# Kernel tuning notes

Measured on AMD Instinct MI355X. Metric: run time of the kernel, lower is better.

## Reference

```python
import jax, jax.numpy as jnp
import numpy as np
import math

D = 1024
H = 16
NEG = -10000.0


def _layernorm(x, g, b, eps=1e-6):
    mu = x.mean(-1, keepdims=True)
    var = ((x - mu) ** 2).mean(-1, keepdims=True)
    return (x - mu) / jnp.sqrt(var + eps) * g + b


def _gelu(x):
    return x * 0.5 * (1.0 + jax.lax.erf(x / math.sqrt(2.0)))


def _split_heads(x):
    N, L, _ = x.shape
    return x.reshape(N, L, H, D // H).transpose(0, 2, 1, 3)  # (N,H,L,d)


def _attention(q, k, v, mask):
    # q,k,v: (N,Lq/Lk,D); mask: (N,1,Lq,Lk) of 0/1 or None
    d = D // H
    qh, kh, vh = _split_heads(q), _split_heads(k), _split_heads(v)
    scores = jnp.einsum('bhqd,bhkd->bhqk', qh, kh) / math.sqrt(d)
    if mask is not None:
        scores = scores + (1.0 - mask) * NEG
    probs = jax.nn.softmax(scores, axis=-1)
    ctx = jnp.einsum('bhqk,bhkd->bhqd', probs, vh)
    N, _, Lq, _ = ctx.shape
    ctx = ctx.transpose(0, 2, 1, 3).reshape(N, Lq, D)
    return ctx, scores.mean(1)  # attention_vis = masked scaled scores averaged over heads


def setup_inputs() -> dict:
    key = jax.random.key(0)
    ks = jax.random.split(key, 16)
    N, Lt, Lv = 16, 512, 512
    w = lambda k: (jax.random.normal(k, (D, D), jnp.float32) * 0.02)
    inp = {
        'dec_hidden_states': jax.random.normal(ks[0], (N, Lt, D), jnp.float32),
        'dec_mask': jnp.ones((N, Lt), jnp.float32),
        'enc_outputs': jax.random.normal(ks[1], (N, Lv, D), jnp.float32),
        'sa_wq': w(ks[2]), 'sa_bq': jnp.zeros((D,), jnp.float32),
        'sa_wk': w(ks[3]), 'sa_bk': jnp.zeros((D,), jnp.float32),
        'sa_wv': w(ks[4]), 'sa_bv': jnp.zeros((D,), jnp.float32),
        'n1_g': jnp.ones((D,), jnp.float32), 'n1_b': jnp.zeros((D,), jnp.float32),
        'ca_wq': w(ks[5]), 'ca_bq': jnp.zeros((D,), jnp.float32),
        'ca_wk': w(ks[6]), 'ca_bk': jnp.zeros((D,), jnp.float32),
        'ca_wv': w(ks[7]), 'ca_bv': jnp.zeros((D,), jnp.float32),
        'n2_g': jnp.ones((D,), jnp.float32), 'n2_b': jnp.zeros((D,), jnp.float32),
        'int_w': w(ks[8]), 'int_b': jnp.zeros((D,), jnp.float32),
        'out_w': w(ks[9]), 'out_b': jnp.zeros((D,), jnp.float32),
        'out_g': jnp.ones((D,), jnp.float32), 'out_beta': jnp.zeros((D,), jnp.float32),
    }
    return inp


def reference(dec_hidden_states, dec_mask, enc_outputs,
              sa_wq, sa_bq, sa_wk, sa_bk, sa_wv, sa_bv, n1_g, n1_b,
              ca_wq, ca_bq, ca_wk, ca_bk, ca_wv, ca_bv, n2_g, n2_b,
              int_w, int_b, out_w, out_b, out_g, out_beta):
    x = dec_hidden_states
    N, Lt, _ = x.shape
    # causal + padding mask: (N,1,Lt) * tril(Lt,Lt) -> (N,Lt,Lt) -> (N,1,Lt,Lt)
    causal = jnp.tril(jnp.ones((Lt, Lt), x.dtype))
    self_mask = (dec_mask[:, None, :] * causal)[:, None, :, :]
    # self attention
    q = x @ sa_wq + sa_bq
    k = x @ sa_wk + sa_bk
    v = x @ sa_wv + sa_bv
    sa_ctx, _ = _attention(q, k, v, self_mask)
    h = _layernorm(sa_ctx + x, n1_g, n1_b)
    # cross attention (no mask)
    cq = h @ ca_wq + ca_bq
    ck = enc_outputs @ ca_wk + ca_bk
    cv = enc_outputs @ ca_wv + ca_bv
    ca_ctx, attention_vis = _attention(cq, ck, cv, None)
    h2 = _layernorm(h + ca_ctx, n2_g, n2_b)
    # intermediate (gelu FFN)
    inter = _gelu(h2 @ int_w + int_b)
    # Output: dense + residual(intermediate itself, as in original) + LayerNorm
    out = _layernorm(inter @ out_w + out_b + inter, out_g, out_beta)
    return out, attention_vis
```

## Files before the change

kernel.cpp:

```cpp
#include <hip/hip_runtime.h>
#include <hip/hip_bf16.h>
#include <math.h>

#define DDIM 1024
#define NH   16
#define LTOK 512
#define NBATCH 16

typedef unsigned short u16;
typedef unsigned short u16x8 __attribute__((ext_vector_type(8)));
typedef unsigned short u16x4 __attribute__((ext_vector_type(4)));
typedef __bf16 bf16x8 __attribute__((ext_vector_type(8)));
typedef float f32x4 __attribute__((ext_vector_type(4)));

typedef __attribute__((address_space(1))) void as1_void;
typedef __attribute__((address_space(3))) void as3_void;

__device__ __forceinline__ void llds16(const u16* g, u16* l) {
    __builtin_amdgcn_global_load_lds((as1_void*)g, (as3_void*)l, 16, 0, 0);
}

__device__ __forceinline__ float bf2f(u16 u) {
    unsigned v = ((unsigned)u) << 16;
    float f; __builtin_memcpy(&f, &v, 4); return f;
}
__device__ __forceinline__ u16 f2bf(float f) {
    unsigned u; __builtin_memcpy(&u, &f, 4);
    u += 0x7fffu + ((u >> 16) & 1u);
    return (u16)(u >> 16);
}

__global__ __launch_bounds__(256) void gemm_bt_kernel(
    const u16* __restrict__ A, int lda, long sA1, long sA2,
    const u16* __restrict__ B, int ldb, long sB1, long sB2,
    u16* __restrict__ C, float* __restrict__ Cf, int ldc, long sC1, long sC2,
    int M, int N, int K, int zdiv,
    const float* __restrict__ bias, float scale, int flags)
{
    __shared__ __align__(16) u16 As[2 * 128 * 32];
    __shared__ __align__(16) u16 Bs[2 * 128 * 32];
    const int BUF = 128 * 32;

    const int z  = blockIdx.y;
    const int zb = z / zdiv, zh = z - zb * zdiv;
    const u16* Ab = A + (long)zb * sA1 + (long)zh * sA2;
    const u16* Bb = B + (long)zb * sB1 + (long)zh * sB2;
    u16*   Cb  = C  ? C  + (long)zb * sC1 + (long)zh * sC2 : nullptr;
    float* Cfb = Cf ? Cf + (long)zb * sC1 + (long)zh * sC2 : nullptr;

    const int tilesN = (N + 127) >> 7;
    const int tilesM = (M + 127) >> 7;
    int tm, tn;
    if ((tilesM & 7) == 0) {
        const int xcd = blockIdx.x & 7, idx = blockIdx.x >> 3;
        const int mg  = tilesM >> 3;
        tm = ((idx % mg) << 3) | xcd;
        tn = idx / mg;
    } else {
        tm = blockIdx.x / tilesN;
        tn = blockIdx.x - tm * tilesN;
    }
    const int m0 = tm << 7, n0 = tn << 7;

    const int tid  = threadIdx.x;
    const int lane = tid & 63;
    const int wave = tid >> 6;
    const int wm = (wave & 1) << 6, wn = (wave >> 1) << 6;
    const int quad = lane >> 4, l16 = lane & 15;

    f32x4 acc[4][4];
#pragma unroll
    for (int i = 0; i < 4; i++)
#pragma unroll
        for (int j = 0; j < 4; j++) acc[i][j] = (f32x4){0.f, 0.f, 0.f, 0.f};

    const int lrA = (wave << 5) + (lane >> 2);
    const int lc  = (lane & 3) << 3;
    int ra0 = m0 + lrA;      if (ra0 > M - 1) ra0 = M - 1;
    int ra1 = m0 + lrA + 16; if (ra1 > M - 1) ra1 = M - 1;
    int rb0 = n0 + lrA;      if (rb0 > N - 1) rb0 = N - 1;
    int rb1 = n0 + lrA + 16; if (rb1 > N - 1) rb1 = N - 1;
    const u16* gA0 = Ab + (long)ra0 * lda + lc;
    const u16* gA1 = Ab + (long)ra1 * lda + lc;
    const u16* gB0 = Bb + (long)rb0 * ldb + lc;
    const u16* gB1 = Bb + (long)rb1 * ldb + lc;
    u16* lA0 = As + ((wave << 5) +  0) * 32;
    u16* lA1 = As + ((wave << 5) + 16) * 32;
    u16* lB0 = Bs + ((wave << 5) +  0) * 32;
    u16* lB1 = Bs + ((wave << 5) + 16) * 32;

    llds16(gA0, lA0);
    llds16(gA1, lA1);
    llds16(gB0, lB0);
    llds16(gB1, lB1);
    __syncthreads();

    int cur = 0;
    for (int k0 = 0; k0 < K; k0 += 32) {
        const int nxt = cur ^ 1;
        if (k0 + 32 < K) {
            llds16(gA0 + k0 + 32, lA0 + nxt * BUF);
            llds16(gA1 + k0 + 32, lA1 + nxt * BUF);
            llds16(gB0 + k0 + 32, lB0 + nxt * BUF);
            llds16(gB1 + k0 + 32, lB1 + nxt * BUF);
        }

        const u16* Ac = As + cur * BUF;
        const u16* Bc = Bs + cur * BUF;
        bf16x8 af[4], bfr[4];
#pragma unroll
        for (int t = 0; t < 4; t++)
            af[t] = *(const bf16x8*)(Ac + (wm + t * 16 + l16) * 32 + quad * 8);
#pragma unroll
        for (int t = 0; t < 4; t++)
            bfr[t] = *(const bf16x8*)(Bc + (wn + t * 16 + l16) * 32 + quad * 8);
#pragma unroll
        for (int i = 0; i < 4; i++)
#pragma unroll
            for (int j = 0; j < 4; j++)
                acc[i][j] = __builtin_amdgcn_mfma_f32_16x16x32_bf16(
                    af[i], bfr[j], acc[i][j], 0, 0, 0);

        __syncthreads();
        cur = nxt;
    }

#pragma unroll
    for (int j = 0; j < 4; j++) {
        int col  = n0 + wn + j * 16 + l16;
        int colc = col < N ? col : N - 1;
        float bv = bias ? bias[colc] : 0.f;
#pragma unroll
        for (int i = 0; i < 4; i++) {
#pragma unroll
            for (int r = 0; r < 4; r++) {
                int row = m0 + wm + i * 16 + quad * 4 + r;
                float v = acc[i][j][r] * scale + bv;
                if (flags & 1)
                    v = 0.5f * v * (1.f + erff(v * 0.70710678118654752f));
                if (row < M && col < N) {
                    if (Cfb) Cfb[(long)row * ldc + col] = v;
                    else     Cb [(long)row * ldc + col] = f2bf(v);
                }
            }
        }
    }
}

__global__ __launch_bounds__(256, 4) void flash_kernel(
    const u16* __restrict__ Q, const u16* __restrict__ K,
    const u16* __restrict__ VT, u16* __restrict__ O,
    const float* __restrict__ mask, int causal, int ldq, int ldk)
{
    __shared__ __align__(16) u16 Ks[128 * 72];
    __shared__ __align__(16) u16 Vs[64 * 136];
    const int tid  = threadIdx.x;
    const int wave = tid >> 6, lane = tid & 63;
    const int quad = lane >> 4, l16 = lane & 15;
    const int bh = blockIdx.x, qt = blockIdx.y, b = bh >> 4, h = bh & 15;
    const int qbase = qt * 64 + wave * 16;
    const int qrow  = qbase + l16;

    const u16* qp = Q + ((long)b * LTOK + qrow) * ldq + h * 64 + quad * 8;
    bf16x8 aq0 = *(const bf16x8*)(qp);
    bf16x8 aq1 = *(const bf16x8*)(qp + 32);

    f32x4 oacc[4];
#pragma unroll
    for (int jd = 0; jd < 4; jd++) oacc[jd] = (f32x4){0.f, 0.f, 0.f, 0.f};
    float m_st = -3.0e38f;
    float l_st = 0.f;

    const int krow = tid >> 3,       kcol = (tid & 7) << 3;
    const int vrow = tid >> 2,       vcol = (tid & 3) << 3;
    const u16* gK = K + ((long)b * LTOK + krow) * ldk + h * 64 + kcol;
    const u16* gV = VT + ((long)bh * 64 + vrow) * LTOK + vcol;

    const float C1    = 0.125f * 1.44269504088896340736f;
    const float NEGL2 = -10000.0f * 1.44269504088896340736f;

    const int nkt = causal ? ((qt * 64 + 63) >> 7) + 1 : (LTOK >> 7);

    u16x8 KR[4], VR[4];
#pragma unroll
    for (int i = 0; i < 4; i++) KR[i] = *(const u16x8*)(gK + (long)(i * 32) * ldk);
#pragma unroll
    for (int i = 0; i < 4; i++) VR[i] = *(const u16x8*)(gV + i * 32);
#pragma unroll
    for (int i = 0; i < 4; i++)
        *(u16x8*)(Ks + (i * 32 + krow) * 72 + kcol) = KR[i];
#pragma unroll
    for (int i = 0; i < 4; i++)
        *(u16x8*)(Vs + vrow * 136 + i * 32 + vcol) = VR[i];
    __syncthreads();

    for (int kt = 0; kt < nkt; kt++) {
        const int k0 = kt << 7;
        const bool more = (kt + 1 < nkt);

        if (more) {
            const int kn = k0 + 128;
#pragma unroll
            for (int i = 0; i < 4; i++)
                KR[i] = *(const u16x8*)(gK + (long)(kn + i * 32) * ldk);
#pragma unroll
            for (int i = 0; i < 4; i++)
                VR[i] = *(const u16x8*)(gV + kn + i * 32);
        }

        f32x4 s[8];
#pragma unroll
        for (int j = 0; j < 8; j++) {
            bf16x8 bk0 = *(const bf16x8*)(Ks + (j * 16 + l16) * 72 + quad * 8);
            bf16x8 bk1 = *(const bf16x8*)(Ks + (j * 16 + l16) * 72 + 32 + quad * 8);
            f32x4 z = (f32x4){0.f, 0.f, 0.f, 0.f};
            z = __builtin_amdgcn_mfma_f32_16x16x32_bf16(bk0, aq0, z, 0, 0, 0);
            s[j] = __builtin_amdgcn_mfma_f32_16x16x32_bf16(bk1, aq1, z, 0, 0, 0);
        }

        float tm0 = -3.0e38f, tm1 = -3.0e38f, tm2 = -3.0e38f, tm3 = -3.0e38f;
#pragma unroll
        for (int j = 0; j < 8; j++) {
            if (causal) {
                f32x4 m4 = *(const f32x4*)(mask + (long)b * LTOK + k0 + j * 16 + quad * 4);
#pragma unroll
                for (int r = 0; r < 4; r++) {
                    int key = k0 + j * 16 + quad * 4 + r;
                    float ad = (key <= qrow) ? fmaf(m4[r], -NEGL2, NEGL2) : NEGL2;
                    s[j][r] = fmaf(s[j][r], C1, ad);
                }
            } else {
#pragma unroll
                for (int r = 0; r < 4; r++) s[j][r] *= C1;
            }
            tm0 = fmaxf(tm0, s[j][0]); tm1 = fmaxf(tm1, s[j][1]);
            tm2 = fmaxf(tm2, s[j][2]); tm3 = fmaxf(tm3, s[j][3]);
        }
        float tmax = fmaxf(fmaxf(tm0, tm1), fmaxf(tm2, tm3));
        tmax = fmaxf(tmax, __shfl_xor(tmax, 16));
        tmax = fmaxf(tmax, __shfl_xor(tmax, 32));

        float mnew  = fmaxf(m_st, tmax);
        float alpha = __builtin_amdgcn_exp2f(m_st - mnew);
        m_st = mnew;

        float rs0 = 0.f, rs1 = 0.f, rs2 = 0.f, rs3 = 0.f;
        unsigned pk[8][2];
#pragma unroll
        for (int j = 0; j < 8; j++) {
            float p0 = __builtin_amdgcn_exp2f(s[j][0] - mnew);
            float p1 = __builtin_amdgcn_exp2f(s[j][1] - mnew);
            float p2 = __builtin_amdgcn_exp2f(s[j][2] - mnew);
            float p3 = __builtin_amdgcn_exp2f(s[j][3] - mnew);
            rs0 += p0; rs1 += p1; rs2 += p2; rs3 += p3;
            asm("v_cvt_pk_bf16_f32 %0, %1, %2" : "=v"(pk[j][0]) : "v"(p0), "v"(p1));
            asm("v_cvt_pk_bf16_f32 %0, %1, %2" : "=v"(pk[j][1]) : "v"(p2), "v"(p3));
        }
        float rsum = (rs0 + rs1) + (rs2 + rs3);
        rsum += __shfl_xor(rsum, 16);
        rsum += __shfl_xor(rsum, 32);
        l_st = l_st * alpha + rsum;

#pragma unroll
        for (int jd = 0; jd < 4; jd++) oacc[jd] *= alpha;

#pragma unroll
        for (int kk = 0; kk < 4; kk++) {
            unsigned wv[4] = { pk[2 * kk][0], pk[2 * kk][1],
                               pk[2 * kk + 1][0], pk[2 * kk + 1][1] };
            bf16x8 bp; __builtin_memcpy(&bp, wv, 16);
#pragma unroll
            for (int jd = 0; jd < 4; jd++) {
                const u16* vb = Vs + (jd * 16 + l16) * 136 + kk * 32 + quad * 4;
                u16 va[8];
                *(u16x4*)(va)     = *(const u16x4*)(vb);
                *(u16x4*)(va + 4) = *(const u16x4*)(vb + 16);
                bf16x8 av; __builtin_memcpy(&av, va, 16);
                oacc[jd] = __builtin_amdgcn_mfma_f32_16x16x32_bf16(av, bp, oacc[jd], 0, 0, 0);
            }
        }

        if (more) {
            __syncthreads();
#pragma unroll
            for (int i = 0; i < 4; i++)
                *(u16x8*)(Ks + (i * 32 + krow) * 72 + kcol) = KR[i];
#pragma unroll
            for (int i = 0; i < 4; i++)
                *(u16x8*)(Vs + vrow * 136 + i * 32 + vcol) = VR[i];
            __syncthreads();
        }
    }

    float linv = 1.f / l_st;
    long obase = ((long)b * LTOK + qrow) * DDIM + h * 64;
#pragma unroll
    for (int jd = 0; jd < 4; jd++) {
        u16x4 ov;
#pragma unroll
        for (int r = 0; r < 4; r++) ov[r] = f2bf(oacc[jd][r] * linv);
        *(u16x4*)(O + obase + jd * 16 + quad * 4) = ov;
    }
}

__global__ __launch_bounds__(256) void add_ln_kernel(
    const u16* __restrict__ a, const u16* __restrict__ b,
    const float* __restrict__ b32,
    const float* __restrict__ g, const float* __restrict__ bt,
    u16* __restrict__ o, float* __restrict__ of)
{
    long row = blockIdx.x;
    int tid = threadIdx.x;
    __shared__ float red[4];
    const u16* ar = a + row * DDIM;
    float xv[4]; float s = 0.f;
#pragma unroll
    for (int i = 0; i < 4; i++) {
        int c = tid + 256 * i;
        float sum = bf2f(ar[c]) + (b32 ? b32[row * DDIM + c] : bf2f(b[row * DDIM + c]));
        xv[i] = fminf(fmaxf(sum, -1.0e18f), 1.0e18f);
        s += xv[i];
    }
#pragma unroll
    for (int ofs = 32; ofs >= 1; ofs >>= 1) s += __shfl_xor(s, ofs);
    int wave = tid >> 6, lane = tid & 63;
    if (lane == 0) red[wave] = s;
    __syncthreads();
    float mu = (red[0] + red[1] + red[2] + red[3]) * (1.f / 1024.f);
    __syncthreads();
    float v = 0.f;
#pragma unroll
    for (int i = 0; i < 4; i++) { float d = xv[i] - mu; v += d * d; }
#pragma unroll
    for (int ofs = 32; ofs >= 1; ofs >>= 1) v += __shfl_xor(v, ofs);
    if (lane == 0) red[wave] = v;
    __syncthreads();
    float var = (red[0] + red[1] + red[2] + red[3]) * (1.f / 1024.f);
    float inv = rsqrtf(var + 1e-6f);
#pragma unroll
    for (int i = 0; i < 4; i++) {
        int c = tid + 256 * i;
        float r = (xv[i] - mu) * inv * g[c] + bt[c];
        if (of) of[row * DDIM + c] = r;
        else    o [row * DDIM + c] = f2bf(r);
    }
}

__global__ __launch_bounds__(256) void cvt_kernel(
    const float* __restrict__ src, u16* __restrict__ dst)
{
    long i = ((long)blockIdx.x * 256 + threadIdx.x) * 8;
    u16x8 o;
#pragma unroll
    for (int j = 0; j < 8; j++) o[j] = f2bf(src[i + j]);
    *(u16x8*)(dst + i) = o;
}

__global__ __launch_bounds__(256) void wt_kernel(
    const float* w0, const float* w1, const float* w2, const float* w3,
    const float* w4, const float* w5, const float* w6, const float* w7,
    u16* __restrict__ wt)
{
    const float* srcs[8] = {w0, w1, w2, w3, w4, w5, w6, w7};
    const float* w = srcs[blockIdx.z];
    u16* o = wt + (long)blockIdx.z * DDIM * DDIM;
    __shared__ u16 t[32][33];
    int tx = threadIdx.x & 31, ty = threadIdx.x >> 5;
    int c0 = blockIdx.x << 5, r0 = blockIdx.y << 5;
#pragma unroll
    for (int i = 0; i < 4; i++)
        t[ty + 8 * i][tx] = f2bf(w[(long)(r0 + ty + 8 * i) * DDIM + c0 + tx]);
    __syncthreads();
#pragma unroll
    for (int i = 0; i < 4; i++)
        o[(long)(c0 + ty + 8 * i) * DDIM + r0 + tx] = t[tx][ty + 8 * i];
}

__global__ __launch_bounds__(256) void biascat_kernel(
    const float* __restrict__ b0, const float* __restrict__ b1,
    const float* __restrict__ b2, float* __restrict__ dst)
{
    int i = blockIdx.x * 256 + threadIdx.x;
    const float* s = (i < 1024) ? b0 : (i < 2048) ? b1 : b2;
    dst[i] = s[i & 1023];
}

__global__ __launch_bounds__(256) void vtrans_kernel(
    const u16* __restrict__ v, u16* __restrict__ vt, int ldv)
{
    int bh = blockIdx.y; int b = bh >> 4, h = bh & 15;
    int k0 = blockIdx.x << 5;
    __shared__ __align__(16) u16 t[32 * 72];
    int kk = threadIdx.x >> 3, c = (threadIdx.x & 7) << 3;
    u16x8 val = *(const u16x8*)(v + ((long)b * LTOK + k0 + kk) * ldv + h * 64 + c);
    *(u16x8*)(t + kk * 72 + c) = val;
    __syncthreads();
    int dd = threadIdx.x >> 2, k2 = (threadIdx.x & 3) << 3;
    u16x8 o;
#pragma unroll
    for (int j = 0; j < 8; j++) o[j] = t[(k2 + j) * 72 + dd];
    *(u16x8*)(vt + ((long)bh * 64 + dd) * LTOK + k0 + k2) = o;
}

extern "C" void kernel_launch(void* const* d_in, const int* in_sizes, int n_in,
                              void* d_out, int out_size, void* d_ws, size_t ws_size,
                              hipStream_t stream)
{
    const float* x     = (const float*)d_in[0];
    const float* dmsk  = (const float*)d_in[1];
    const float* enc   = (const float*)d_in[2];
    const float* sa_wq = (const float*)d_in[3];  const float* sa_bq = (const float*)d_in[4];
    const float* sa_wk = (const float*)d_in[5];  const float* sa_bk = (const float*)d_in[6];
    const float* sa_wv = (const float*)d_in[7];  const float* sa_bv = (const float*)d_in[8];
    const float* n1_g  = (const float*)d_in[9];  const float* n1_b  = (const float*)d_in[10];
    const float* ca_wq = (const float*)d_in[11]; const float* ca_bq = (const float*)d_in[12];
    const float* ca_wk = (const float*)d_in[13]; const float* ca_bk = (const float*)d_in[14];
    const float* ca_wv = (const float*)d_in[15]; const float* ca_bv = (const float*)d_in[16];
    const float* n2_g  = (const float*)d_in[17]; const float* n2_b  = (const float*)d_in[18];
    const float* int_w = (const float*)d_in[19]; const float* int_b = (const float*)d_in[20];
    const float* out_w = (const float*)d_in[21]; const float* out_b = (const float*)d_in[22];
    const float* out_g = (const float*)d_in[23]; const float* out_bt= (const float*)d_in[24];

    float* outp = (float*)d_out;
    float* visp = outp + (long)NBATCH * LTOK * DDIM;

    const size_t WTB  = (size_t)8 * DDIM * DDIM * 2;
    const size_t BUF1 = (size_t)LTOK * DDIM * 2;
    int cb = 16;
    while (cb > 1 && WTB + (size_t)cb * 7 * BUF1 + 32768 > ws_size)
        cb >>= 1;

    char* ws = (char*)d_ws;
    size_t off = 0;
    auto alloc = [&](size_t bytes) -> u16* {
        u16* p = (u16*)(ws + off);
        off += (bytes + 255) & ~(size_t)255;
        return p;
    };
    u16* Xb  = alloc((size_t)cb * BUF1);
    u16* Eb  = alloc((size_t)cb * BUF1);
    u16* Q3  = alloc((size_t)cb * 3 * BUF1);
    u16* Vt  = alloc((size_t)cb * BUF1);
    u16* Cx  = alloc((size_t)cb * BUF1);
    u16* WT  = alloc(WTB);
    float* biasQKV = (float*)alloc(3072 * sizeof(float));
    float* biasKV  = (float*)alloc(2048 * sizeof(float));

    u16* Wsaq = WT + 0L * DDIM * DDIM;
    u16* Wcaq = WT + 3L * DDIM * DDIM;
    u16* Wcak = WT + 4L * DDIM * DDIM;
    u16* Wint = WT + 6L * DDIM * DDIM;
    u16* Wout = WT + 7L * DDIM * DDIM;

    auto gemm = [&](const u16* A, int lda, long sA1, long sA2,
                    const u16* B, int ldb, long sB1, long sB2,
                    u16* C, float* Cf, int ldc, long sC1, long sC2,
                    int M, int N, int K, int Z, int zdiv,
                    const float* bias, float scale, int flags) {
        int tM = (M + 127) / 128, tN = (N + 127) / 128;
        gemm_bt_kernel<<<dim3(tM * tN, Z), dim3(256), 0, stream>>>(
            A, lda, sA1, sA2, B, ldb, sB1, sB2, C, Cf, ldc, sC1, sC2,
            M, N, K, zdiv, bias, scale, flags);
    };

    const long SLD = (long)LTOK * DDIM;
    const long SSC = (long)LTOK * LTOK;

    wt_kernel<<<dim3(32, 32, 8), dim3(256), 0, stream>>>(
        sa_wq, sa_wk, sa_wv, ca_wq, ca_wk, ca_wv, int_w, out_w, WT);
    biascat_kernel<<<dim3(12), dim3(256), 0, stream>>>(sa_bq, sa_bk, sa_bv, biasQKV);
    biascat_kernel<<<dim3(8),  dim3(256), 0, stream>>>(ca_bk, ca_bv, ca_bv, biasKV);

    for (int b0 = 0; b0 < NBATCH; b0 += cb) {
        const float* xc = x   + (long)b0 * SLD;
        const float* ec = enc + (long)b0 * SLD;
        const int M = cb * LTOK;
        const int Z = cb * NH;
        const int cvtg = (int)(((long)M * DDIM) / (256 * 8));

        u16* h   = Xb;
        u16* CQ  = Q3;
        u16* CKV = Q3 + (size_t)cb * LTOK * DDIM;
        u16* I   = Q3;
        u16* G   = Q3 + (size_t)cb * LTOK * DDIM;
        u16* h2  = Eb;

        cvt_kernel<<<dim3(cvtg), dim3(256), 0, stream>>>(xc, Xb);
        cvt_kernel<<<dim3(cvtg), dim3(256), 0, stream>>>(ec, Eb);

        gemm(Xb, DDIM, 0, 0, Wsaq, DDIM, 0, 0, Q3, nullptr, 3 * DDIM, 0, 0,
             M, 3 * DDIM, DDIM, 1, 1, biasQKV, 1.f, 0);
        vtrans_kernel<<<dim3(16, Z), dim3(256), 0, stream>>>(Q3 + 2 * DDIM, Vt, 3 * DDIM);

        flash_kernel<<<dim3(Z, 8), dim3(256), 0, stream>>>(
            Q3, Q3 + DDIM, Vt, Cx, dmsk + (long)b0 * LTOK, 1, 3 * DDIM, 3 * DDIM);

        add_ln_kernel<<<dim3(M), dim3(256), 0, stream>>>(
            Cx, nullptr, xc, n1_g, n1_b, h, nullptr);

        gemm(h, DDIM, 0, 0, Wcaq, DDIM, 0, 0, CQ, nullptr, DDIM, 0, 0,
             M, DDIM, DDIM, 1, 1, ca_bq, 1.f, 0);
        gemm(Eb, DDIM, 0, 0, Wcak, DDIM, 0, 0, CKV, nullptr, 2 * DDIM, 0, 0,
             M, 2 * DDIM, DDIM, 1, 1, biasKV, 1.f, 0);

        gemm(CQ, DDIM, SLD, 0, CKV, 2 * DDIM, (long)LTOK * 2 * DDIM, 0,
             nullptr, visp + (long)b0 * SSC, LTOK, SSC, 0,
             LTOK, LTOK, DDIM, cb, 1, nullptr, 1.f / 128.f, 0);

        vtrans_kernel<<<dim3(16, Z), dim3(256), 0, stream>>>(CKV + DDIM, Vt, 2 * DDIM);
        flash_kernel<<<dim3(Z, 8), dim3(256), 0, stream>>>(
            CQ, CKV, Vt, Cx, nullptr, 0, DDIM, 2 * DDIM);

        add_ln_kernel<<<dim3(M), dim3(256), 0, stream>>>(
            h, Cx, nullptr, n2_g, n2_b, h2, nullptr);

        gemm(h2, DDIM, 0, 0, Wint, DDIM, 0, 0, I, nullptr, DDIM, 0, 0,
             M, DDIM, DDIM, 1, 1, int_b, 1.f, 1);
        gemm(I, DDIM, 0, 0, Wout, DDIM, 0, 0, G, nullptr, DDIM, 0, 0,
             M, DDIM, DDIM, 1, 1, out_b, 1.f, 0);
        add_ln_kernel<<<dim3(M), dim3(256), 0, stream>>>(
            G, I, nullptr, out_g, out_bt, nullptr, outp + (long)b0 * SLD);
    }
}
```

Measured before the change: 577.9 us.

## Template GEMM on pipeline depth by grid size and vectorize epilogue stores

The GEMM kernel is templated on a buffering mode: single-buffered for large grids (less LDS, more occupancy), double-buffered for medium grids, and triple-buffered with explicit vmcnt waits for small grids. It also drops the boundary clamps, assuming dimensions are multiples of 128. MFMA operands are swapped so each lane holds four consecutive columns, which lets the epilogue write vectorized 4-wide stores and load bias as a vector. The risks are the loss of edge handling for non-aligned shapes and extra synchronization in the single-buffer path.

Result: no change. 586.3 us (+1.5%).

```diff
diff --git a/kernel.cpp b/kernel.cpp
--- a/kernel.cpp
+++ b/kernel.cpp
@@ -30,6 +30,7 @@
     return (u16)(u >> 16);
 }
 
+template<int MODE>
 __global__ __launch_bounds__(256) void gemm_bt_kernel(
     const u16* __restrict__ A, int lda, long sA1, long sA2,
     const u16* __restrict__ B, int ldb, long sB1, long sB2,
@@ -37,9 +38,10 @@
     int M, int N, int K, int zdiv,
     const float* __restrict__ bias, float scale, int flags)
 {
-    __shared__ __align__(16) u16 As[2 * 128 * 32];
-    __shared__ __align__(16) u16 Bs[2 * 128 * 32];
-    const int BUF = 128 * 32;
+    constexpr int NB   = (MODE == 0) ? 1 : (MODE == 1 ? 2 : 3);
+    constexpr int BUFE = 128 * 32;
+    __shared__ __align__(16) u16 As[NB * BUFE];
+    __shared__ __align__(16) u16 Bs[NB * BUFE];
 
     const int z  = blockIdx.y;
     const int zb = z / zdiv, zh = z - zb * zdiv;
@@ -48,8 +50,8 @@
     u16*   Cb  = C  ? C  + (long)zb * sC1 + (long)zh * sC2 : nullptr;
     float* Cfb = Cf ? Cf + (long)zb * sC1 + (long)zh * sC2 : nullptr;
 
-    const int tilesN = (N + 127) >> 7;
-    const int tilesM = (M + 127) >> 7;
+    const int tilesN = N >> 7;
+    const int tilesM = M >> 7;
     int tm, tn;
     if ((tilesM & 7) == 0) {
         const int xcd = blockIdx.x & 7, idx = blockIdx.x >> 3;
@@ -76,37 +78,24 @@
 
     const int lrA = (wave << 5) + (lane >> 2);
     const int lc  = (lane & 3) << 3;
-    int ra0 = m0 + lrA;      if (ra0 > M - 1) ra0 = M - 1;
-    int ra1 = m0 + lrA + 16; if (ra1 > M - 1) ra1 = M - 1;
-    int rb0 = n0 + lrA;      if (rb0 > N - 1) rb0 = N - 1;
-    int rb1 = n0 + lrA + 16; if (rb1 > N - 1) rb1 = N - 1;
-    const u16* gA0 = Ab + (long)ra0 * lda + lc;
-    const u16* gA1 = Ab + (long)ra1 * lda + lc;
-    const u16* gB0 = Bb + (long)rb0 * ldb + lc;
-    const u16* gB1 = Bb + (long)rb1 * ldb + lc;
+    const u16* gA0 = Ab + (long)(m0 + lrA) * lda + lc;
+    const u16* gA1 = Ab + (long)(m0 + lrA + 16) * lda + lc;
+    const u16* gB0 = Bb + (long)(n0 + lrA) * ldb + lc;
+    const u16* gB1 = Bb + (long)(n0 + lrA + 16) * ldb + lc;
     u16* lA0 = As + ((wave << 5) +  0) * 32;
     u16* lA1 = As + ((wave << 5) + 16) * 32;
     u16* lB0 = Bs + ((wave << 5) +  0) * 32;
     u16* lB1 = Bs + ((wave << 5) + 16) * 32;
 
-    llds16(gA0, lA0);
-    llds16(gA1, lA1);
-    llds16(gB0, lB0);
-    llds16(gB1, lB1);
-    __syncthreads();
-
-    int cur = 0;
-    for (int k0 = 0; k0 < K; k0 += 32) {
-        const int nxt = cur ^ 1;
-        if (k0 + 32 < K) {
-            llds16(gA0 + k0 + 32, lA0 + nxt * BUF);
-            llds16(gA1 + k0 + 32, lA1 + nxt * BUF);
-            llds16(gB0 + k0 + 32, lB0 + nxt * BUF);
-            llds16(gB1 + k0 + 32, lB1 + nxt * BUF);
-        }
-
-        const u16* Ac = As + cur * BUF;
-        const u16* Bc = Bs + cur * BUF;
+    auto STAGE = [&](int bi, int k0) {
+        llds16(gA0 + k0, lA0 + bi * BUFE);
+        llds16(gA1 + k0, lA1 + bi * BUFE);
+        llds16(gB0 + k0, lB0 + bi * BUFE);
+        llds16(gB1 + k0, lB1 + bi * BUFE);
+    };
+    auto COMPUTE = [&](int bi) {
+        const u16* Ac = As + bi * BUFE;
+        const u16* Bc = Bs + bi * BUFE;
         bf16x8 af[4], bfr[4];
 #pragma unroll
         for (int t = 0; t < 4; t++)
@@ -119,29 +108,72 @@
 #pragma unroll
             for (int j = 0; j < 4; j++)
                 acc[i][j] = __builtin_amdgcn_mfma_f32_16x16x32_bf16(
-                    af[i], bfr[j], acc[i][j], 0, 0, 0);
-
+                    bfr[j], af[i], acc[i][j], 0, 0, 0);
+    };
+
+    if (MODE == 0) {
+        for (int k0 = 0; k0 < K; k0 += 32) {
+            __syncthreads();
+            STAGE(0, k0);
+            __syncthreads();
+            COMPUTE(0);
+        }
+    } else if (MODE == 1) {
+        STAGE(0, 0);
         __syncthreads();
-        cur = nxt;
-    }
-
-#pragma unroll
-    for (int j = 0; j < 4; j++) {
-        int col  = n0 + wn + j * 16 + l16;
-        int colc = col < N ? col : N - 1;
-        float bv = bias ? bias[colc] : 0.f;
-#pragma unroll
-        for (int i = 0; i < 4; i++) {
+        int cur = 0;
+        for (int k0 = 0; k0 < K; k0 += 32) {
+            const int nxt = cur ^ 1;
+            if (k0 + 32 < K) STAGE(nxt, k0 + 32);
+            COMPUTE(cur);
+            __syncthreads();
+            cur = nxt;
+        }
+    } else {
+        STAGE(0, 0);
+        STAGE(1, 32);
+        int cur = 0;
+        for (int k0 = 0; k0 < K; k0 += 32) {
+            if (k0 + 32 < K) {
+                asm volatile("s_waitcnt vmcnt(4) lgkmcnt(0)" ::: "memory");
+            } else {
+                asm volatile("s_waitcnt vmcnt(0) lgkmcnt(0)" ::: "memory");
+            }
+            __builtin_amdgcn_sched_barrier(0);
+            __builtin_amdgcn_s_barrier();
+            __builtin_amdgcn_sched_barrier(0);
+            if (k0 + 64 < K) {
+                int pre = cur + 2; if (pre >= 3) pre -= 3;
+                STAGE(pre, k0 + 64);
+            }
+            COMPUTE(cur);
+            cur = (cur == 2) ? 0 : cur + 1;
+        }
+    }
+
+#pragma unroll
+    for (int i = 0; i < 4; i++) {
+        const long row = m0 + wm + i * 16 + l16;
+#pragma unroll
+        for (int j = 0; j < 4; j++) {
+            const int col = n0 + wn + j * 16 + quad * 4;
+            f32x4 bv = bias ? *(const f32x4*)(bias + col)
+                            : (f32x4){0.f, 0.f, 0.f, 0.f};
+            f32x4 v4;
 #pragma unroll
             for (int r = 0; r < 4; r++) {
-                int row = m0 + wm + i * 16 + quad * 4 + r;
-                float v = acc[i][j][r] * scale + bv;
+                float v = acc[i][j][r] * scale + bv[r];
                 if (flags & 1)
                     v = 0.5f * v * (1.f + erff(v * 0.70710678118654752f));
-                if (row < M && col < N) {
-                    if (Cfb) Cfb[(long)row * ldc + col] = v;
-                    else     Cb [(long)row * ldc + col] = f2bf(v);
-                }
+                v4[r] = v;
+            }
+            if (Cfb) {
+                *(f32x4*)(Cfb + row * ldc + col) = v4;
+            } else {
+                u16x4 ov;
+#pragma unroll
+                for (int r = 0; r < 4; r++) ov[r] = f2bf(v4[r]);
+                *(u16x4*)(Cb + row * ldc + col) = ov;
             }
         }
     }
@@ -457,10 +489,21 @@
                     u16* C, float* Cf, int ldc, long sC1, long sC2,
                     int M, int N, int K, int Z, int zdiv,
                     const float* bias, float scale, int flags) {
-        int tM = (M + 127) / 128, tN = (N + 127) / 128;
-        gemm_bt_kernel<<<dim3(tM * tN, Z), dim3(256), 0, stream>>>(
-            A, lda, sA1, sA2, B, ldb, sB1, sB2, C, Cf, ldc, sC1, sC2,
-            M, N, K, zdiv, bias, scale, flags);
+        int tM = M / 128, tN = N / 128;
+        long total = (long)tM * tN * Z;
+        dim3 g(tM * tN, Z), blk(256);
+        if (total >= 1536)
+            gemm_bt_kernel<0><<<g, blk, 0, stream>>>(
+                A, lda, sA1, sA2, B, ldb, sB1, sB2, C, Cf, ldc, sC1, sC2,
+                M, N, K, zdiv, bias, scale, flags);
+        else if (total >= 1024)
+            gemm_bt_kernel<1><<<g, blk, 0, stream>>>(
+                A, lda, sA1, sA2, B, ldb, sB1, sB2, C, Cf, ldc, sC1, sC2,
+                M, N, K, zdiv, bias, scale, flags);
+        else
+            gemm_bt_kernel<2><<<g, blk, 0, stream>>>(
+                A, lda, sA1, sA2, B, ldb, sB1, sB2, C, Cf, ldc, sC1, sC2,
+                M, N, K, zdiv, bias, scale, flags);
     };
 
     const long SLD = (long)LTOK * DDIM;
```
